# Performance work log

Measured on AMD Instinct MI355X. Metric: run time of the kernel, lower is better.

The kernel has to match this reference:

```python
import jax, jax.numpy as jnp
import numpy as np

B, N, D = 16, 1369, 1024
HID, NH = 512, 8
SCALE = np.sqrt(D // NH)


def _pos_encoding_2d(n, d):
    ps = int(np.sqrt(n))  # 37; n is a perfect square here
    div = jnp.exp(jnp.arange(0, d // 2, 2, dtype=jnp.float32) * (-np.log(10000.0) / (d // 2)))
    rows = (jnp.arange(n) // ps).astype(jnp.float32)
    cols = (jnp.arange(n) % ps).astype(jnp.float32)
    def interleave(s, c):
        return jnp.stack([s, c], axis=-1).reshape(n, -1)
    half_row = interleave(jnp.sin(rows[:, None] * div), jnp.cos(rows[:, None] * div))
    half_col = interleave(jnp.sin(cols[:, None] * div), jnp.cos(cols[:, None] * div))
    return jnp.concatenate([half_row, half_col], axis=-1)  # [n, d]


def _center_bias(n, strength=0.3):
    ps = int(np.sqrt(n))
    c = ps // 2
    y, x = jnp.meshgrid(jnp.arange(ps, dtype=jnp.float32), jnp.arange(ps, dtype=jnp.float32), indexing='ij')
    d2 = (x - c) ** 2 + (y - c) ** 2
    sigma = ps / 6.0
    return (jnp.exp(-d2 / (2.0 * sigma ** 2)).reshape(-1)) * strength  # [n]


def setup_inputs() -> dict:
    key = jax.random.key(0)
    ks = jax.random.split(key, 16)
    s = 0.02
    return {
        'patch_tokens': jax.random.normal(ks[0], (B, N, D), dtype=jnp.float32),
        'curiosity_score': jax.random.uniform(ks[1], (B,), dtype=jnp.float32),
        'Wq': jax.random.normal(ks[2], (D, D), dtype=jnp.float32) * s,
        'bq': jax.random.uniform(ks[3], (D,), minval=-0.05, maxval=0.05, dtype=jnp.float32),
        'Wk': jax.random.normal(ks[4], (D, D), dtype=jnp.float32) * s,
        'bk': jax.random.uniform(ks[5], (D,), minval=-0.05, maxval=0.05, dtype=jnp.float32),
        'Wv': jax.random.normal(ks[6], (D, D), dtype=jnp.float32) * s,
        'bv': jnp.zeros((D,), dtype=jnp.float32),
        'Wc1': jax.random.normal(ks[7], (1, HID // 8), dtype=jnp.float32) * s,
        'bc1': jnp.zeros((HID // 8,), dtype=jnp.float32),
        'Wc2': jax.random.normal(ks[8], (HID // 8, NH), dtype=jnp.float32) * s,
        'bc2': jnp.zeros((NH,), dtype=jnp.float32),
        'Wp1': jax.random.normal(ks[9], (D, HID), dtype=jnp.float32) * s,
        'bp1': jnp.zeros((HID,), dtype=jnp.float32),
        'Wp2': jax.random.normal(ks[10], (HID, HID // 4), dtype=jnp.float32) * s,
        'bp2': jnp.zeros((HID // 4,), dtype=jnp.float32),
        'adaptive_weight': jnp.float32(0.5),
    }


def reference(patch_tokens, curiosity_score, Wq, bq, Wk, bk, Wv, bv,
              Wc1, bc1, Wc2, bc2, Wp1, bp1, Wp2, bp2, adaptive_weight):
    b, n, d = patch_tokens.shape
    x = patch_tokens + _pos_encoding_2d(n, d)[None]  # [B,N,D]

    q = x @ Wq + bq
    k = x @ Wk + bk
    v = x @ Wv + bv

    scores = jnp.einsum('bqd,bkd->bqk', q, k) / SCALE          # [B,N,N]
    attn = jax.nn.softmax(scores, axis=-1)                     # dropout p=0 / eval
    attended = jnp.einsum('bqk,bkd->bqd', attn, v)             # [B,N,D]

    cb = _center_bias(n)[None]                                 # [1,N]
    VAR_EPS = 1e-6

    pa = attn.mean(axis=1) + cb
    # fallback chain (data-dependent in torch; expressed with jnp.where)
    pa2 = jnp.diagonal(attn, axis1=-2, axis2=-1) + cb
    pa = jnp.where(jnp.var(pa, ddof=1) < VAR_EPS, pa2, pa)
    pa3 = attn.max(axis=-1) + cb
    pa = jnp.where(jnp.var(pa, ddof=1) < VAR_EPS, pa3, pa)
    norms = jnp.linalg.norm(x, axis=-1)
    noise = jax.random.normal(jax.random.key(42), norms.shape, dtype=norms.dtype) * 0.1 * jnp.std(norms, ddof=1)
    pa = jnp.where(jnp.var(pa, ddof=1) < VAR_EPS, norms + noise, pa)

    pa = pa / (pa.sum(axis=-1, keepdims=True) + 1e-8)

    # curiosity modulation
    h = jax.nn.relu(curiosity_score[:, None] @ Wc1 + bc1)
    cm = jax.nn.sigmoid(h @ Wc2 + bc2)                         # [B,NH]
    cw = cm.mean(axis=-1, keepdims=True)                       # [B,1]
    modulated = pa * (1.0 + cw)
    fa = adaptive_weight * modulated + (1.0 - adaptive_weight) * pa

    fa = jnp.clip(fa, 1e-8, None)
    fa = fa / (fa.sum(axis=-1, keepdims=True) + 1e-8)

    weighted = jnp.sum(attended * fa[..., None], axis=1)       # [B,D]
    focal = jax.nn.relu(weighted @ Wp1 + bp1) @ Wp2 + bp2      # [B,HID//4]
    return focal, fa
```

## Files before the change

kernel.cpp:

```cpp
#include <hip/hip_runtime.h>
#include <hip/hip_bf16.h>
#include <cstdint>

#define B_   16
#define N_   1369
#define NP   1536
#define D_   1024
#define NQKV 3072
#define SLD  1568
#define QLD  3104

typedef __bf16 bf16x8_t __attribute__((ext_vector_type(8)));
typedef __bf16 bf16x4_t __attribute__((ext_vector_type(4)));
typedef float  f32x4_t  __attribute__((ext_vector_type(4)));

__device__ __forceinline__ float  bf2f(__bf16 x) { return (float)x; }
__device__ __forceinline__ __bf16 f2bf(float x)  { return (__bf16)x; }

#define GLOAD_LDS16(g, l) __builtin_amdgcn_global_load_lds( \
    (const __attribute__((address_space(1))) void*)(g),     \
    (__attribute__((address_space(3))) void*)(l), 16, 0, 0)

__global__ __launch_bounds__(256)
void pos_kernel(float* __restrict__ pos)
{
    const int idx = blockIdx.x * 256 + threadIdx.x;
    if (idx >= N_ * D_) return;
    const int n = idx >> 10, f = idx & 1023;
    const int row = n / 37, col = n - row * 37;
    const float base = (f < 512) ? (float)row : (float)col;
    const int  t2   = (f & 511) >> 1;
    const float dv  = __expf(-0.03597789207803197f * (float)t2);
    const float ang = base * dv;
    pos[idx] = (f & 1) ? cosf(ang) : sinf(ang);
}

__global__ __launch_bounds__(256)
void addpos_kernel(const float* __restrict__ patch, const float* __restrict__ pos,
                   __bf16* __restrict__ X)
{
    const long tid = (long)blockIdx.x * 256 + threadIdx.x;
    const long e   = tid * 4;
    const int  f   = (int)(e & 1023);
    const long nb  = e >> 10;
    const int  n   = (int)(nb % NP);
    const long b   = nb / NP;
    bf16x4_t o;
    if (n < N_) {
        const float4 p = *(const float4*)(patch + ((b * N_ + n) << 10) + f);
        const float4 q = *(const float4*)(pos + ((long)n << 10) + f);
        o[0] = f2bf(p.x + q.x); o[1] = f2bf(p.y + q.y);
        o[2] = f2bf(p.z + q.z); o[3] = f2bf(p.w + q.w);
    } else {
        o[0] = o[1] = o[2] = o[3] = f2bf(0.f);
    }
    *(bf16x4_t*)(X + e) = o;
}

__global__ __launch_bounds__(256)
void wcast_kernel(const float* __restrict__ W0, const float* __restrict__ W1,
                  const float* __restrict__ W2,
                  __bf16* __restrict__ T0, __bf16* __restrict__ T1, __bf16* __restrict__ T2)
{
    const float* W = blockIdx.z == 0 ? W0 : (blockIdx.z == 1 ? W1 : W2);
    __bf16*      T = blockIdx.z == 0 ? T0 : (blockIdx.z == 1 ? T1 : T2);
    __shared__ float tile[64][65];
    const int o0 = blockIdx.x * 64, i0 = blockIdx.y * 64;
    const int t = threadIdx.x;
    const int tr = t >> 4, tc = (t & 15) * 4;
    #pragma unroll
    for (int rr = 0; rr < 64; rr += 16) {
        float4 v = *(const float4*)(W + (long)(i0 + rr + tr) * 1024 + o0 + tc);
        tile[rr + tr][tc + 0] = v.x; tile[rr + tr][tc + 1] = v.y;
        tile[rr + tr][tc + 2] = v.z; tile[rr + tr][tc + 3] = v.w;
    }
    __syncthreads();
    #pragma unroll
    for (int rr = 0; rr < 64; rr += 16) {
        bf16x4_t o;
        o[0] = f2bf(tile[tc + 0][rr + tr]); o[1] = f2bf(tile[tc + 1][rr + tr]);
        o[2] = f2bf(tile[tc + 2][rr + tr]); o[3] = f2bf(tile[tc + 3][rr + tr]);
        *(bf16x4_t*)(T + (long)(o0 + rr + tr) * 1024 + i0 + tc) = o;
    }
}

__global__ __launch_bounds__(256)
void bcat_kernel(const float* __restrict__ bq, const float* __restrict__ bk,
                 const float* __restrict__ bv, float* __restrict__ bcat)
{
    const int i = blockIdx.x * 256 + threadIdx.x;
    if (i >= NQKV) return;
    const int p = i >> 10, j = i & 1023;
    bcat[i] = p == 0 ? bq[j] : (p == 1 ? bk[j] : bv[j]);
}

template<int HAS_BIAS>
__global__ __launch_bounds__(512, 2)
void gemm256(const __bf16* __restrict__ A, const __bf16* __restrict__ Bt,
             __bf16* __restrict__ C, const float* __restrict__ bias,
             int lda, int ldb, int ldc, int Kd, float scale,
             long sA, long sB, long sC, int tilesN, int tilesPerBatch, int cpx)
{
    __shared__ __bf16 lds[65536];
    const int bid = blockIdx.x;
    const int vt  = (bid & 7) * cpx + (bid >> 3);
    const int bz  = vt / tilesPerBatch;
    const int rem = vt - bz * tilesPerBatch;
    const int ty  = rem / tilesN;
    const int tx  = rem - ty * tilesN;
    A  += (long)bz * sA;  Bt += (long)bz * sB;  C += (long)bz * sC;
    const int m0 = ty * 256, n0 = tx * 256;

    const int t  = threadIdx.x;
    const int w  = t >> 6, l = t & 63;
    const int wr = w >> 2, wc = w & 3;
    const int lr = l & 15, lh = l >> 4;

    const int laneF  = (lr * 64 + ((lh * 16) ^ (((lr >> 3) & 1) << 5))) >> 1;
    const int rstage = w * 16 + (l >> 2);
    const int kstage = ((l & 3) * 8) ^ (((l >> 5) & 1) << 4);

    const __bf16* Ag = A  + (long)(m0 + rstage) * lda + kstage;
    const __bf16* Bg = Bt + (long)(n0 + rstage) * ldb + kstage;
    __bf16* dA = lds + w * 1024;
    __bf16* dB = lds + 16384 + w * 1024;

#define SA_(buf, half, kt) do {                                       \
    const __bf16* g_ = Ag + (long)(half) * 128 * lda + (kt) * 64;     \
    __bf16* d_ = dA + (buf) * 32768 + (half) * 8192;                  \
    GLOAD_LDS16(g_, d_); GLOAD_LDS16(g_ + 32, d_ + 512); } while (0)
#define SB_(buf, half, kt) do {                                       \
    const __bf16* g_ = Bg + (long)(half) * 128 * ldb + (kt) * 64;     \
    __bf16* d_ = dB + (buf) * 32768 + (half) * 8192;                  \
    GLOAD_LDS16(g_, d_); GLOAD_LDS16(g_ + 32, d_ + 512); } while (0)

    f32x4_t acc[8][4] = {};
    bf16x8_t bfr[4][2];
    bf16x8_t aX0, aX1, aX2, aX3, aY0, aY1, aY2, aY3;

#define AREAD_(S0,S1,S2,S3, base, p) do {                                    \
    const __bf16* ap_ = lds + (base) + wr * 8192 + (p) * 2048 + laneF;       \
    S0 = *(const bf16x8_t*)(ap_);                                            \
    S1 = *(const bf16x8_t*)(ap_ + 512);                                      \
    S2 = *(const bf16x8_t*)(ap_ + 1024);                                     \
    S3 = *(const bf16x8_t*)(ap_ + 1536); } while (0)

#define BREAD_(base) do { const __bf16* bp_ = lds + (base) + laneF;                        \
    bfr[0][0] = *(const bf16x8_t*)(bp_);        bfr[0][1] = *(const bf16x8_t*)(bp_ + 512); \
    bfr[1][0] = *(const bf16x8_t*)(bp_ + 1024); bfr[1][1] = *(const bf16x8_t*)(bp_ + 1536);\
    bfr[2][0] = *(const bf16x8_t*)(bp_ + 2048); bfr[2][1] = *(const bf16x8_t*)(bp_ + 2560);\
    bfr[3][0] = *(const bf16x8_t*)(bp_ + 3072); bfr[3][1] = *(const bf16x8_t*)(bp_ + 3584);} while (0)

#define MFMAC_(pp, S0,S1,S2,S3) do {                                                   \
    __builtin_amdgcn_s_setprio(1);                                                     \
    _Pragma("unroll") for (int nn = 0; nn < 4; ++nn)                                   \
      acc[(pp)*2+0][nn] = __builtin_amdgcn_mfma_f32_16x16x32_bf16(S0, bfr[nn][0], acc[(pp)*2+0][nn], 0, 0, 0); \
    _Pragma("unroll") for (int nn = 0; nn < 4; ++nn)                                   \
      acc[(pp)*2+1][nn] = __builtin_amdgcn_mfma_f32_16x16x32_bf16(S2, bfr[nn][0], acc[(pp)*2+1][nn], 0, 0, 0); \
    _Pragma("unroll") for (int nn = 0; nn < 4; ++nn)                                   \
      acc[(pp)*2+0][nn] = __builtin_amdgcn_mfma_f32_16x16x32_bf16(S1, bfr[nn][1], acc[(pp)*2+0][nn], 0, 0, 0); \
    _Pragma("unroll") for (int nn = 0; nn < 4; ++nn)                                   \
      acc[(pp)*2+1][nn] = __builtin_amdgcn_mfma_f32_16x16x32_bf16(S3, bfr[nn][1], acc[(pp)*2+1][nn], 0, 0, 0); \
    __builtin_amdgcn_s_setprio(0); } while (0)

#define SBAR_ __builtin_amdgcn_sched_barrier(0)
#define BAR_  __builtin_amdgcn_s_barrier()

    const int NT = Kd >> 6;
    SA_(0, 0, 0); SA_(0, 1, 0); SB_(0, 0, 0); SB_(0, 1, 0);
    SB_(1, 0, 1); SB_(1, 1, 1);
    asm volatile("s_waitcnt vmcnt(4)" ::: "memory");
    BAR_;

    for (int tk = 0; tk < NT; ++tk) {
        const int c  = tk & 1, o = c ^ 1;
        const int t1 = (tk + 1 < NT) ? tk + 1 : NT - 1;
        const int t2 = (tk + 2 < NT) ? tk + 2 : NT - 1;
        const int st = (tk + 2 < NT);
        const int cbase = c * 32768;
        const int cbB   = cbase + 16384 + wc * 4096;
        AREAD_(aX0, aX1, aX2, aX3, cbase, 0);
        BREAD_(cbB);
        SBAR_;
        AREAD_(aY0, aY1, aY2, aY3, cbase, 1);
        SA_(o, 0, t1);
        SBAR_; BAR_;
        MFMAC_(0, aX0, aX1, aX2, aX3);
        BAR_;
        AREAD_(aX0, aX1, aX2, aX3, cbase, 2);
        SA_(o, 1, t1);
        SBAR_; BAR_;
        MFMAC_(1, aY0, aY1, aY2, aY3);
        BAR_;
        AREAD_(aY0, aY1, aY2, aY3, cbase, 3);
        SB_(c, 0, t2);
        SBAR_; BAR_;
        MFMAC_(2, aX0, aX1, aX2, aX3);
        BAR_;
        SB_(c, 1, t2);
        SBAR_; BAR_;
        MFMAC_(3, aY0, aY1, aY2, aY3);
        if (st) { asm volatile("s_waitcnt vmcnt(4)" ::: "memory"); }
        else    { asm volatile("s_waitcnt vmcnt(0)" ::: "memory"); }
        BAR_;
    }

    #pragma unroll
    for (int mi = 0; mi < 8; ++mi) {
        const int row = m0 + wr * 128 + mi * 16 + lh * 4;
        #pragma unroll
        for (int nn = 0; nn < 4; ++nn) {
            const int col = n0 + wc * 64 + nn * 16 + lr;
            const float bb = HAS_BIAS ? bias[col] : 0.0f;
            #pragma unroll
            for (int q = 0; q < 4; ++q)
                C[(long)(row + q) * ldc + col] = f2bf(acc[mi][nn][q] * scale + bb);
        }
    }
#undef SA_
#undef SB_
#undef AREAD_
#undef BREAD_
#undef MFMAC_
#undef SBAR_
#undef BAR_
}

__global__ __launch_bounds__(256)
void softmax_kernel(__bf16* __restrict__ S)
{
    const int wid  = threadIdx.x >> 6;
    const int lane = threadIdx.x & 63;
    const int q    = blockIdx.x * 4 + wid;
    const int b    = blockIdx.y;
    if (q >= N_) return;
    __bf16* row = S + ((long)b * NP + q) * SLD;
    float v[24];
    float m = -1e30f;
    #pragma unroll
    for (int j = 0; j < 3; ++j) {
        const int k0 = j * 512 + lane * 8;
        bf16x8_t raw = *(const bf16x8_t*)(row + k0);
        #pragma unroll
        for (int i = 0; i < 8; ++i) {
            const float x = (k0 + i < N_) ? bf2f(raw[i]) : -1e30f;
            v[j * 8 + i] = x; m = fmaxf(m, x);
        }
    }
    #pragma unroll
    for (int o = 32; o; o >>= 1) m = fmaxf(m, __shfl_xor(m, o));
    float s = 0.f;
    #pragma unroll
    for (int j = 0; j < 3; ++j) {
        const int k0 = j * 512 + lane * 8;
        #pragma unroll
        for (int i = 0; i < 8; ++i) {
            if (k0 + i < N_) { const float e = __expf(v[j * 8 + i] - m); v[j * 8 + i] = e; s += e; }
            else             v[j * 8 + i] = 0.f;
        }
    }
    #pragma unroll
    for (int o = 32; o; o >>= 1) s += __shfl_xor(s, o);
    const float inv = 1.f / s;
    #pragma unroll
    for (int j = 0; j < 3; ++j) {
        const int k0 = j * 512 + lane * 8;
        bf16x8_t o8;
        #pragma unroll
        for (int i = 0; i < 8; ++i) o8[i] = f2bf(v[j * 8 + i] * inv);
        *(bf16x8_t*)(row + k0) = o8;
    }
}

template<int WEIGHTED>
__global__ __launch_bounds__(256)
void colsum_kernel(const __bf16* __restrict__ attn, const float* __restrict__ wv,
                   float* __restrict__ out)
{
    const int t = threadIdx.x;
    if (t >= 192) return;
    const int b  = blockIdx.y;
    const int q0 = blockIdx.x * 16;
    const int q1 = (q0 + 16 < N_) ? q0 + 16 : N_;
    const int k8 = t * 8;
    float s[8] = {};
    const __bf16* base = attn + (long)b * NP * SLD + k8;
    for (int q = q0; q < q1; ++q) {
        bf16x8_t v = *(const bf16x8_t*)(base + (long)q * SLD);
        const float wq = WEIGHTED ? wv[b * NP + q] : 1.0f;
        #pragma unroll
        for (int i = 0; i < 8; ++i) s[i] += wq * bf2f(v[i]);
    }
    #pragma unroll
    for (int i = 0; i < 8; ++i) atomicAdd(out + b * NP + k8 + i, s[i]);
}

__global__ __launch_bounds__(256)
void fa_kernel(const float* __restrict__ pa_raw, const float* __restrict__ curiosity,
               const float* __restrict__ Wc1, const float* __restrict__ bc1,
               const float* __restrict__ Wc2, const float* __restrict__ bc2,
               const float* __restrict__ aw_p,
               float* __restrict__ fa_ws, float* __restrict__ out_fa)
{
    const int b = blockIdx.x, t = threadIdx.x;
    __shared__ float hsh[64];
    __shared__ float red[8];
    __shared__ float cwsh;
    if (t < 64) hsh[t] = fmaxf(0.f, curiosity[b] * Wc1[t] + bc1[t]);
    __syncthreads();
    if (t < 8) {
        float a = bc2[t];
        for (int j = 0; j < 64; ++j) a += hsh[j] * Wc2[j * 8 + t];
        red[t] = 1.f / (1.f + __expf(-a));
    }
    __syncthreads();
    if (t == 0) {
        float cw = 0.f;
        for (int i = 0; i < 8; ++i) cw += red[i];
        cwsh = cw * 0.125f;
    }
    __syncthreads();
    const float aw   = aw_p[0];
    const float modf = 1.f + aw * cwsh;
    const float sig  = 37.f / 6.f;
    const float inv2s2 = 1.f / (2.f * sig * sig);
    float pv[6];
    float s1 = 0.f;
    #pragma unroll
    for (int i = 0; i < 6; ++i) {
        const int k = t + i * 256;
        float p = 0.f;
        if (k < N_) {
            const int y = k / 37, x = k - y * 37;
            const float d2 = (float)((x - 18) * (x - 18) + (y - 18) * (y - 18));
            const float cb = 0.3f * __expf(-d2 * inv2s2);
            p = pa_raw[b * NP + k] * (1.f / 1369.f) + cb;
        }
        pv[i] = p; s1 += p;
    }
    #pragma unroll
    for (int o = 32; o; o >>= 1) s1 += __shfl_xor(s1, o);
    __syncthreads();
    if (!(t & 63)) red[t >> 6] = s1;
    __syncthreads();
    s1 = red[0] + red[1] + red[2] + red[3];
    const float inv1 = 1.f / (s1 + 1e-8f);
    float s2 = 0.f;
    #pragma unroll
    for (int i = 0; i < 6; ++i) {
        const int k = t + i * 256;
        if (k < N_) {
            const float f = fmaxf(pv[i] * inv1 * modf, 1e-8f);
            pv[i] = f; s2 += f;
        }
    }
    #pragma unroll
    for (int o = 32; o; o >>= 1) s2 += __shfl_xor(s2, o);
    if (!(t & 63)) red[4 + (t >> 6)] = s2;
    __syncthreads();
    s2 = red[4] + red[5] + red[6] + red[7];
    const float inv2 = 1.f / (s2 + 1e-8f);
    #pragma unroll
    for (int i = 0; i < 6; ++i) {
        const int k = t + i * 256;
        if (k < N_) {
            const float f = pv[i] * inv2;
            fa_ws[b * NP + k]  = f;
            out_fa[b * N_ + k] = f;
        }
    }
}

__global__ __launch_bounds__(256)
void weighted_kernel(const float* __restrict__ g, const __bf16* __restrict__ V,
                     int ldv, float* __restrict__ wout)
{
    const int b  = blockIdx.y;
    const int k0 = blockIdx.x * 86;
    const int k1 = (k0 + 86 < N_) ? k0 + 86 : N_;
    const int d  = threadIdx.x * 4;
    float a0 = 0, a1 = 0, a2 = 0, a3 = 0;
    const __bf16* vb = V + (long)b * NP * ldv + d;
    for (int k = k0; k < k1; ++k) {
        const float gv = g[b * NP + k];
        bf16x4_t vv = *(const bf16x4_t*)(vb + (long)k * ldv);
        a0 += gv * bf2f(vv[0]); a1 += gv * bf2f(vv[1]);
        a2 += gv * bf2f(vv[2]); a3 += gv * bf2f(vv[3]);
    }
    atomicAdd(wout + b * D_ + d + 0, a0);
    atomicAdd(wout + b * D_ + d + 1, a1);
    atomicAdd(wout + b * D_ + d + 2, a2);
    atomicAdd(wout + b * D_ + d + 3, a3);
}

__global__ __launch_bounds__(256)
void focal1_kernel(const float* __restrict__ weighted, const float* __restrict__ Wp1,
                   const float* __restrict__ bp1, float* __restrict__ h)
{
    const int b = blockIdx.y, jc = blockIdx.x;
    const int t = threadIdx.x;
    const int jl = t >> 2, part = t & 3;
    const int j = jc * 64 + jl;
    const float* wb = weighted + b * 1024 + part * 256;
    const float* wp = Wp1 + (long)(part * 256) * 512 + j;
    float a = 0.f;
    #pragma unroll 8
    for (int d = 0; d < 256; ++d) a += wb[d] * wp[(long)d * 512];
    a += __shfl_xor(a, 1);
    a += __shfl_xor(a, 2);
    if (part == 0) h[b * 512 + j] = fmaxf(a + bp1[j], 0.f);
}

__global__ __launch_bounds__(128)
void focal2_kernel(const float* __restrict__ h, const float* __restrict__ Wp2,
                   const float* __restrict__ bp2, float* __restrict__ out)
{
    const int b = blockIdx.x, o = threadIdx.x;
    __shared__ float hs[512];
    for (int i = o; i < 512; i += 128) hs[i] = h[b * 512 + i];
    __syncthreads();
    float a = bp2[o];
    #pragma unroll 8
    for (int j = 0; j < 512; ++j) a += hs[j] * Wp2[j * 128 + o];
    out[b * 128 + o] = a;
}

extern "C" void kernel_launch(void* const* d_in, const int* in_sizes, int n_in,
                              void* d_out, int out_size, void* d_ws, size_t ws_size,
                              hipStream_t stream)
{
    const float* patch     = (const float*)d_in[0];
    const float* curiosity = (const float*)d_in[1];
    const float* Wq  = (const float*)d_in[2];
    const float* bq  = (const float*)d_in[3];
    const float* Wk  = (const float*)d_in[4];
    const float* bk  = (const float*)d_in[5];
    const float* Wv  = (const float*)d_in[6];
    const float* bv  = (const float*)d_in[7];
    const float* Wc1 = (const float*)d_in[8];
    const float* bc1 = (const float*)d_in[9];
    const float* Wc2 = (const float*)d_in[10];
    const float* bc2 = (const float*)d_in[11];
    const float* Wp1 = (const float*)d_in[12];
    const float* bp1 = (const float*)d_in[13];
    const float* Wp2 = (const float*)d_in[14];
    const float* bp2 = (const float*)d_in[15];
    const float* aw  = (const float*)d_in[16];
    float* out = (float*)d_out;

    char* ws = (char*)d_ws;
    size_t off = 0;
    auto alloc = [&](size_t bytes) -> char* {
        char* p = ws + off;
        off += (bytes + 255) & ~(size_t)255;
        return p;
    };
    float*  pos  = (float*) alloc((size_t)N_ * D_ * 4);
    __bf16* X    = (__bf16*)alloc((size_t)B_ * NP * D_ * 2);
    __bf16* WT   = (__bf16*)alloc((size_t)3 * D_ * D_ * 2);
    const size_t S_BYTES = (size_t)B_ * NP * SLD * 2;
    if (off < S_BYTES) off = S_BYTES;
    __bf16* S    = (__bf16*)ws;
    __bf16* QKV  = (__bf16*)alloc((size_t)B_ * NP * QLD * 2);
    float*  pa   = (float*) alloc((size_t)B_ * NP * 4);
    float*  faw  = (float*) alloc((size_t)B_ * NP * 4);
    float*  gbuf = (float*) alloc((size_t)B_ * NP * 4);
    float*  wsum = (float*) alloc((size_t)B_ * D_ * 4);
    float*  bcat = (float*) alloc((size_t)NQKV * 4);
    float*  hbuf = (float*) alloc((size_t)B_ * 512 * 4);

    (void)hipMemsetAsync(pa,   0, (size_t)B_ * NP * 4, stream);
    (void)hipMemsetAsync(gbuf, 0, (size_t)B_ * NP * 4, stream);
    (void)hipMemsetAsync(wsum, 0, (size_t)B_ * D_ * 4, stream);

    pos_kernel<<<(N_ * D_ + 255) / 256, 256, 0, stream>>>(pos);
    addpos_kernel<<<(int)((size_t)B_ * NP * D_ / 4 / 256), 256, 0, stream>>>(patch, pos, X);
    {
        dim3 g(16, 16, 3);
        wcast_kernel<<<g, 256, 0, stream>>>(Wq, Wk, Wv,
                                            WT, WT + D_ * D_, WT + 2 * D_ * D_);
    }
    bcat_kernel<<<(NQKV + 255) / 256, 256, 0, stream>>>(bq, bk, bv, bcat);
    {
        const int nwg = 96 * 12;
        gemm256<1><<<nwg, 512, 0, stream>>>(X, WT, QKV, bcat,
                                            D_, D_, QLD, D_, 1.0f,
                                            0, 0, 0, 12, nwg, nwg / 8);
    }
    {
        const int nwg = 36 * B_;
        gemm256<0><<<nwg, 512, 0, stream>>>(QKV, QKV + D_, S, nullptr,
                                            QLD, QLD, SLD, D_,
                                            0.08838834764831845f,
                                            (long)NP * QLD, (long)NP * QLD,
                                            (long)NP * SLD, 6, 36, nwg / 8);
    }
    {
        dim3 g((N_ + 3) / 4, B_);
        softmax_kernel<<<g, 256, 0, stream>>>(S);
    }
    {
        dim3 g(86, B_);
        colsum_kernel<0><<<g, 256, 0, stream>>>(S, nullptr, pa);
    }
    fa_kernel<<<B_, 256, 0, stream>>>(pa, curiosity, Wc1, bc1, Wc2, bc2, aw,
                                      faw, out + B_ * 128);
    {
        dim3 g(86, B_);
        colsum_kernel<1><<<g, 256, 0, stream>>>(S, faw, gbuf);
    }
    {
        dim3 g(16, B_);
        weighted_kernel<<<g, 256, 0, stream>>>(gbuf, QKV + 2 * D_, QLD, wsum);
    }
    {
        dim3 g(8, B_);
        focal1_kernel<<<g, 256, 0, stream>>>(wsum, Wp1, bp1, hbuf);
    }
    focal2_kernel<<<B_, 128, 0, stream>>>(hbuf, Wp2, bp2, out);
}
```

Measured before the change: 562.2 us.

## Replace interleaved 8-phase GEMM pipeline with simple double-buffered prefetch loop

Replaces the finely interleaved GEMM main loop, which split each k-tile into four MFMA phases with barriers and staggered A/B loads two tiles ahead, with a plain double-buffered loop. The new loop issues all loads for the next tile up front, reads all A/B fragments from LDS, runs every MFMA, then waits for memory and synchronises once per tile. This cuts barrier count and scheduling complexity, but exposes LDS read latency before the MFMAs, shortens prefetch depth, and raises register pressure from holding 24 fragments.

Measured after the change: 560.4 us. About the same (-0.3%).

```diff
diff --git a/kernel.cpp b/kernel.cpp
--- a/kernel.cpp
+++ b/kernel.cpp
@@ -135,74 +135,44 @@
     GLOAD_LDS16(g_, d_); GLOAD_LDS16(g_ + 32, d_ + 512); } while (0)
 
     f32x4_t acc[8][4] = {};
-    bf16x8_t bfr[4][2];
-    bf16x8_t aX0, aX1, aX2, aX3, aY0, aY1, aY2, aY3;
-
-#define AREAD_(S0,S1,S2,S3, base, p) do {                                    \
-    const __bf16* ap_ = lds + (base) + wr * 8192 + (p) * 2048 + laneF;       \
-    S0 = *(const bf16x8_t*)(ap_);                                            \
-    S1 = *(const bf16x8_t*)(ap_ + 512);                                      \
-    S2 = *(const bf16x8_t*)(ap_ + 1024);                                     \
-    S3 = *(const bf16x8_t*)(ap_ + 1536); } while (0)
-
-#define BREAD_(base) do { const __bf16* bp_ = lds + (base) + laneF;                        \
-    bfr[0][0] = *(const bf16x8_t*)(bp_);        bfr[0][1] = *(const bf16x8_t*)(bp_ + 512); \
-    bfr[1][0] = *(const bf16x8_t*)(bp_ + 1024); bfr[1][1] = *(const bf16x8_t*)(bp_ + 1536);\
-    bfr[2][0] = *(const bf16x8_t*)(bp_ + 2048); bfr[2][1] = *(const bf16x8_t*)(bp_ + 2560);\
-    bfr[3][0] = *(const bf16x8_t*)(bp_ + 3072); bfr[3][1] = *(const bf16x8_t*)(bp_ + 3584);} while (0)
-
-#define MFMAC_(pp, S0,S1,S2,S3) do {                                                   \
-    __builtin_amdgcn_s_setprio(1);                                                     \
-    _Pragma("unroll") for (int nn = 0; nn < 4; ++nn)                                   \
-      acc[(pp)*2+0][nn] = __builtin_amdgcn_mfma_f32_16x16x32_bf16(S0, bfr[nn][0], acc[(pp)*2+0][nn], 0, 0, 0); \
-    _Pragma("unroll") for (int nn = 0; nn < 4; ++nn)                                   \
-      acc[(pp)*2+1][nn] = __builtin_amdgcn_mfma_f32_16x16x32_bf16(S2, bfr[nn][0], acc[(pp)*2+1][nn], 0, 0, 0); \
-    _Pragma("unroll") for (int nn = 0; nn < 4; ++nn)                                   \
-      acc[(pp)*2+0][nn] = __builtin_amdgcn_mfma_f32_16x16x32_bf16(S1, bfr[nn][1], acc[(pp)*2+0][nn], 0, 0, 0); \
-    _Pragma("unroll") for (int nn = 0; nn < 4; ++nn)                                   \
-      acc[(pp)*2+1][nn] = __builtin_amdgcn_mfma_f32_16x16x32_bf16(S3, bfr[nn][1], acc[(pp)*2+1][nn], 0, 0, 0); \
-    __builtin_amdgcn_s_setprio(0); } while (0)
-
-#define SBAR_ __builtin_amdgcn_sched_barrier(0)
-#define BAR_  __builtin_amdgcn_s_barrier()
 
     const int NT = Kd >> 6;
     SA_(0, 0, 0); SA_(0, 1, 0); SB_(0, 0, 0); SB_(0, 1, 0);
-    SB_(1, 0, 1); SB_(1, 1, 1);
-    asm volatile("s_waitcnt vmcnt(4)" ::: "memory");
-    BAR_;
+    asm volatile("s_waitcnt vmcnt(0)" ::: "memory");
+    __builtin_amdgcn_s_barrier();
 
     for (int tk = 0; tk < NT; ++tk) {
-        const int c  = tk & 1, o = c ^ 1;
-        const int t1 = (tk + 1 < NT) ? tk + 1 : NT - 1;
-        const int t2 = (tk + 2 < NT) ? tk + 2 : NT - 1;
-        const int st = (tk + 2 < NT);
+        const int c = tk & 1, o = c ^ 1;
         const int cbase = c * 32768;
-        const int cbB   = cbase + 16384 + wc * 4096;
-        AREAD_(aX0, aX1, aX2, aX3, cbase, 0);
-        BREAD_(cbB);
-        SBAR_;
-        AREAD_(aY0, aY1, aY2, aY3, cbase, 1);
-        SA_(o, 0, t1);
-        SBAR_; BAR_;
-        MFMAC_(0, aX0, aX1, aX2, aX3);
-        BAR_;
-        AREAD_(aX0, aX1, aX2, aX3, cbase, 2);
-        SA_(o, 1, t1);
-        SBAR_; BAR_;
-        MFMAC_(1, aY0, aY1, aY2, aY3);
-        BAR_;
-        AREAD_(aY0, aY1, aY2, aY3, cbase, 3);
-        SB_(c, 0, t2);
-        SBAR_; BAR_;
-        MFMAC_(2, aX0, aX1, aX2, aX3);
-        BAR_;
-        SB_(c, 1, t2);
-        SBAR_; BAR_;
-        MFMAC_(3, aY0, aY1, aY2, aY3);
-        if (st) { asm volatile("s_waitcnt vmcnt(4)" ::: "memory"); }
-        else    { asm volatile("s_waitcnt vmcnt(0)" ::: "memory"); }
-        BAR_;
+        if (tk + 1 < NT) {
+            SA_(o, 0, tk + 1); SA_(o, 1, tk + 1);
+            SB_(o, 0, tk + 1); SB_(o, 1, tk + 1);
+        }
+        const __bf16* bp = lds + cbase + 16384 + wc * 4096 + laneF;
+        const __bf16* ap = lds + cbase + wr * 8192 + laneF;
+        bf16x8_t bf0[4], bf1[4], af0[8], af1[8];
+        #pragma unroll
+        for (int nn = 0; nn < 4; ++nn) bf0[nn] = *(const bf16x8_t*)(bp + nn * 1024);
+        #pragma unroll
+        for (int mi = 0; mi < 8; ++mi) af0[mi] = *(const bf16x8_t*)(ap + mi * 1024);
+        #pragma unroll
+        for (int nn = 0; nn < 4; ++nn) bf1[nn] = *(const bf16x8_t*)(bp + nn * 1024 + 512);
+        #pragma unroll
+        for (int mi = 0; mi < 8; ++mi) af1[mi] = *(const bf16x8_t*)(ap + mi * 1024 + 512);
+        __builtin_amdgcn_s_setprio(1);
+        #pragma unroll
+        for (int mi = 0; mi < 8; ++mi)
+            #pragma unroll
+            for (int nn = 0; nn < 4; ++nn)
+                acc[mi][nn] = __builtin_amdgcn_mfma_f32_16x16x32_bf16(af0[mi], bf0[nn], acc[mi][nn], 0, 0, 0);
+        #pragma unroll
+        for (int mi = 0; mi < 8; ++mi)
+            #pragma unroll
+            for (int nn = 0; nn < 4; ++nn)
+                acc[mi][nn] = __builtin_amdgcn_mfma_f32_16x16x32_bf16(af1[mi], bf1[nn], acc[mi][nn], 0, 0, 0);
+        __builtin_amdgcn_s_setprio(0);
+        asm volatile("s_waitcnt vmcnt(0)" ::: "memory");
+        __builtin_amdgcn_s_barrier();
     }
 
     #pragma unroll
@@ -219,11 +189,6 @@
     }
 #undef SA_
 #undef SB_
-#undef AREAD_
-#undef BREAD_
-#undef MFMAC_
-#undef SBAR_
-#undef BAR_
 }
 
 __global__ __launch_bounds__(256)
```
